# Kernel optimization log

Measured on AMD Instinct MI355X. Metric: run time of the kernel, lower is better.

Reference implementation:

```python
import jax, jax.numpy as jnp
import numpy as np

N_EMBD = 1024
N_HEAD = 16
HEAD_SIZE = N_EMBD // N_HEAD
D_FF = 4 * N_EMBD
B, T = 4, 2048
EPS = 1e-5


def _layernorm(x, w, b):
    mu = jnp.mean(x, axis=-1, keepdims=True)
    var = jnp.mean(jnp.square(x - mu), axis=-1, keepdims=True)
    return (x - mu) * jax.lax.rsqrt(var + EPS) * w + b


def setup_inputs() -> dict:
    key = jax.random.key(0)
    ks = jax.random.split(key, 12)
    s = 0.02
    x = jax.random.normal(ks[0], (B, T, N_EMBD), dtype=jnp.float32)
    # right-padded prefix mask: lengths in [T//2, T] -> no all-masked causal rows
    lengths = jax.random.randint(ks[1], (B,), T // 2, T + 1)
    key_padding_mask = jnp.arange(T)[None, :] < lengths[:, None]  # [B,T] bool, True=keep
    wq = jax.random.normal(ks[2], (N_EMBD, N_HEAD, HEAD_SIZE), dtype=jnp.float32) * s
    wk = jax.random.normal(ks[3], (N_EMBD, N_HEAD, HEAD_SIZE), dtype=jnp.float32) * s
    wv = jax.random.normal(ks[4], (N_EMBD, N_HEAD, HEAD_SIZE), dtype=jnp.float32) * s
    proj_w = jax.random.normal(ks[5], (N_EMBD, N_EMBD), dtype=jnp.float32) * s
    proj_b = jnp.zeros((N_EMBD,), dtype=jnp.float32)
    ff_w1 = jax.random.normal(ks[6], (N_EMBD, D_FF), dtype=jnp.float32) * s
    ff_b1 = jnp.zeros((D_FF,), dtype=jnp.float32)
    ff_w2 = jax.random.normal(ks[7], (D_FF, N_EMBD), dtype=jnp.float32) * s
    ff_b2 = jnp.zeros((N_EMBD,), dtype=jnp.float32)
    ln1_w = jnp.ones((N_EMBD,), dtype=jnp.float32)
    ln1_b = jnp.zeros((N_EMBD,), dtype=jnp.float32)
    ln2_w = jnp.ones((N_EMBD,), dtype=jnp.float32)
    ln2_b = jnp.zeros((N_EMBD,), dtype=jnp.float32)
    return dict(x=x, key_padding_mask=key_padding_mask, wq=wq, wk=wk, wv=wv,
                proj_w=proj_w, proj_b=proj_b, ff_w1=ff_w1, ff_b1=ff_b1,
                ff_w2=ff_w2, ff_b2=ff_b2, ln1_w=ln1_w, ln1_b=ln1_b,
                ln2_w=ln2_w, ln2_b=ln2_b)


def reference(x, key_padding_mask, wq, wk, wv, proj_w, proj_b,
              ff_w1, ff_b1, ff_w2, ff_b2, ln1_w, ln1_b, ln2_w, ln2_b):
    Bn, Tn, C = x.shape
    m = key_padding_mask.astype(x.dtype)  # [B,T]
    # --- attention sublayer ---
    h = _layernorm(x, ln1_w, ln1_b) * m[..., None]
    q = jnp.einsum('btc,chd->bhtd', h, wq)
    k = jnp.einsum('btc,chd->bhtd', h, wk)
    v = jnp.einsum('btc,chd->bhtd', h, wv)
    # NOTE: original scales by full embed dim C**-0.5, not head_size
    scores = jnp.einsum('bhtd,bhsd->bhts', q, k) * (C ** -0.5)
    causal = jnp.tril(jnp.ones((Tn, Tn), dtype=bool))
    mask = causal[None, None, :, :] & key_padding_mask[:, None, None, :]
    scores = jnp.where(mask, scores, -jnp.inf)
    wei = jax.nn.softmax(scores, axis=-1)
    out = jnp.einsum('bhts,bhsd->bthd', wei, v).reshape(Bn, Tn, C)
    x = x + out @ proj_w + proj_b
    # --- feedforward sublayer ---
    h2 = _layernorm(x, ln2_w, ln2_b) * m[..., None]
    ff = jax.nn.relu(h2 @ ff_w1 + ff_b1) @ ff_w2 + ff_b2
    x = (x + ff) * m[..., None]
    return x
```

## Files before the change

kernel.cpp:

```cpp
#include <hip/hip_runtime.h>
#include <math.h>

typedef float f32x4 __attribute__((ext_vector_type(4)));
typedef float f4 __attribute__((ext_vector_type(4)));
typedef __bf16 bf16x8 __attribute__((ext_vector_type(8)));
typedef __bf16 bf16x4 __attribute__((ext_vector_type(4)));

#define GLOBAL_AS __attribute__((address_space(1)))
#define LDS_AS __attribute__((address_space(3)))

__global__ __launch_bounds__(256) void mask_canon(const unsigned char* __restrict__ raw,
                                                  float* __restrict__ msk, int n) {
    int i = blockIdx.x * 256 + threadIdx.x;
    if (i >= n) return;
    unsigned int w0 = *(const unsigned int*)raw;
    float v;
    if (w0 == 0x01010101u)       v = raw[i] ? 1.f : 0.f;
    else if (w0 == 0x3f800000u)  v = ((const float*)raw)[i];
    else                         v = ((const int*)raw)[i] ? 1.f : 0.f;
    msk[i] = v;
}

__global__ __launch_bounds__(256) void lens_kernel(const float* __restrict__ msk,
                                                   float* __restrict__ lens) {
    int b = blockIdx.x, tid = threadIdx.x;
    float s = 0.f;
    for (int i = tid; i < 2048; i += 256) s += msk[b * 2048 + i];
#pragma unroll
    for (int off = 1; off < 64; off <<= 1) s += __shfl_xor(s, off);
    __shared__ float red[4];
    int wave = tid >> 6, lane = tid & 63;
    if (lane == 0) red[wave] = s;
    __syncthreads();
    if (tid == 0) lens[b] = red[0] + red[1] + red[2] + red[3];
}

__global__ __launch_bounds__(256) void tcvt(const float* __restrict__ src,
                                            __bf16* __restrict__ dst, int K, int N) {
    __shared__ float tile[32][33];
    int n0 = blockIdx.x * 32, k0 = blockIdx.y * 32;
    int tx = threadIdx.x & 31, ty = threadIdx.x >> 5;
#pragma unroll
    for (int i = 0; i < 4; ++i)
        tile[ty + 8 * i][tx] = src[(long)(k0 + ty + 8 * i) * N + n0 + tx];
    __syncthreads();
#pragma unroll
    for (int i = 0; i < 4; ++i)
        dst[(long)(n0 + ty + 8 * i) * K + k0 + tx] = (__bf16)tile[tx][ty + 8 * i];
}

__global__ __launch_bounds__(256) void ln_kernel(const float* __restrict__ x,
                                                 const float* __restrict__ w,
                                                 const float* __restrict__ bsc,
                                                 const float* __restrict__ msk,
                                                 __bf16* __restrict__ out) {
    long row = blockIdx.x;
    int tid = threadIdx.x;
    f4 xv = *(const f4*)(x + row * 1024 + tid * 4);
    float s = xv[0] + xv[1] + xv[2] + xv[3];
    float sq = xv[0] * xv[0] + xv[1] * xv[1] + xv[2] * xv[2] + xv[3] * xv[3];
#pragma unroll
    for (int off = 1; off < 64; off <<= 1) {
        s += __shfl_xor(s, off);
        sq += __shfl_xor(sq, off);
    }
    __shared__ float red[2][4];
    int wave = tid >> 6, lane = tid & 63;
    if (lane == 0) { red[0][wave] = s; red[1][wave] = sq; }
    __syncthreads();
    s = red[0][0] + red[0][1] + red[0][2] + red[0][3];
    sq = red[1][0] + red[1][1] + red[1][2] + red[1][3];
    float mu = s * (1.0f / 1024.0f);
    float var = sq * (1.0f / 1024.0f) - mu * mu;
    float rs = rsqrtf(var + 1e-5f);
    float mv = msk[row];
    f4 wv = *(const f4*)(w + tid * 4);
    f4 bv = *(const f4*)(bsc + tid * 4);
    bf16x4 ov;
#pragma unroll
    for (int j = 0; j < 4; ++j)
        ov[j] = (__bf16)(((xv[j] - mu) * rs * wv[j] + bv[j]) * mv);
    *(bf16x4*)(out + row * 1024 + tid * 4) = ov;
}

template <int EP>
__global__ __launch_bounds__(512, 2) void gemm_bt8(const __bf16* __restrict__ A,
                                                   const __bf16* __restrict__ B,
                                                   int K, int N, void* __restrict__ Cout,
                                                   const float* __restrict__ bias) {
    __shared__ __bf16 AB[2][2][256 * 64];
    int tid = threadIdx.x;
    int wave = tid >> 6, lane = tid & 63;
    int l15 = lane & 15, quad = lane >> 4;
    int r8 = l15 & 7;
    int wm = wave >> 2, wn = wave & 3;
    long rowBase = (long)blockIdx.x * 256;
    long colBase = (long)blockIdx.y * 256;
    const __bf16* Ab = A + rowBase * K;
    const __bf16* Bb = B + colBase * K;
    int srow = lane >> 3;
    int scol = ((lane & 7) ^ srow) * 8;
    f32x4 acc[8][4] = {};

#define STAGE2(DST, GB, seg0, kt_)                                                         \
    do {                                                                                   \
        _Pragma("unroll") for (int j = 0; j < 2; ++j) {                                    \
            int s_ = wave * 4 + (seg0) + j;                                                \
            const __bf16* g_ = (GB) + (long)(s_ * 8 + srow) * K + (kt_) + scol;            \
            __builtin_amdgcn_global_load_lds((const GLOBAL_AS void*)g_,                    \
                                             (LDS_AS void*)((char*)(DST) + s_ * 1024), 16, \
                                             0, 0);                                        \
        }                                                                                  \
    } while (0)

#define RDA(mh)                                                                      \
    do {                                                                             \
        _Pragma("unroll") for (int mi = 0; mi < 4; ++mi) {                           \
            int row_ = wm * 128 + (mh) * 64 + mi * 16 + l15;                         \
            af[mi][0] = *(const bf16x8*)(Ac + row_ * 64 + ((quad ^ r8) << 3));       \
            af[mi][1] = *(const bf16x8*)(Ac + row_ * 64 + (((4 + quad) ^ r8) << 3)); \
        }                                                                            \
    } while (0)

#define RDB(h)                                                                              \
    do {                                                                                    \
        _Pragma("unroll") for (int ni = 0; ni < 2; ++ni) {                                  \
            int row_ = wn * 64 + ((h) * 2 + ni) * 16 + l15;                                 \
            bfr[h][ni][0] = *(const bf16x8*)(Bc + row_ * 64 + ((quad ^ r8) << 3));          \
            bfr[h][ni][1] = *(const bf16x8*)(Bc + row_ * 64 + (((4 + quad) ^ r8) << 3));    \
        }                                                                                   \
    } while (0)

#define MM(mh, nh)                                                                          \
    do {                                                                                    \
        __builtin_amdgcn_s_setprio(1);                                                      \
        _Pragma("unroll") for (int mi = 0; mi < 4; ++mi) {                                  \
            _Pragma("unroll") for (int ni = 0; ni < 2; ++ni) {                              \
                acc[(mh) * 4 + mi][(nh) * 2 + ni] = __builtin_amdgcn_mfma_f32_16x16x32_bf16(\
                    af[mi][0], bfr[nh][ni][0], acc[(mh) * 4 + mi][(nh) * 2 + ni], 0, 0, 0); \
                acc[(mh) * 4 + mi][(nh) * 2 + ni] = __builtin_amdgcn_mfma_f32_16x16x32_bf16(\
                    af[mi][1], bfr[nh][ni][1], acc[(mh) * 4 + mi][(nh) * 2 + ni], 0, 0, 0); \
            }                                                                               \
        }                                                                                   \
        __builtin_amdgcn_s_setprio(0);                                                      \
    } while (0)

    STAGE2(&AB[0][0][0], Ab, 0, 0);
    STAGE2(&AB[0][0][0], Ab, 2, 0);
    STAGE2(&AB[0][1][0], Bb, 0, 0);
    STAGE2(&AB[0][1][0], Bb, 2, 0);

    int cur = 0;
    bf16x8 af[4][2], bfr[2][2][2];
    for (int kt = 0; kt < K; kt += 64) {
        const bool lastt = (kt + 64 >= K);
        const __bf16* Ac = &AB[cur][0][0];
        const __bf16* Bc = &AB[cur][1][0];
        __bf16* An = &AB[cur ^ 1][0][0];
        __bf16* Bn = &AB[cur ^ 1][1][0];
        if (!lastt) {
            STAGE2(An, Ab, 0, kt + 64);
            __asm__ volatile("s_waitcnt vmcnt(2)" ::: "memory");
        } else {
            __asm__ volatile("s_waitcnt vmcnt(0)" ::: "memory");
        }
        __asm__ volatile("s_barrier" ::: "memory");
        RDA(0);
        RDB(0);
        MM(0, 0);
        if (!lastt) STAGE2(An, Ab, 2, kt + 64);
        RDB(1);
        MM(0, 1);
        if (!lastt) STAGE2(Bn, Bb, 0, kt + 64);
        RDA(1);
        MM(1, 1);
        if (!lastt) STAGE2(Bn, Bb, 2, kt + 64);
        MM(1, 0);
        __asm__ volatile("s_barrier" ::: "memory");
        cur ^= 1;
    }
#undef STAGE2
#undef RDA
#undef RDB
#undef MM

#pragma unroll
    for (int mi = 0; mi < 8; ++mi) {
#pragma unroll
        for (int r = 0; r < 4; ++r) {
            long gr = rowBase + wm * 128 + mi * 16 + quad * 4 + r;
#pragma unroll
            for (int ni = 0; ni < 4; ++ni) {
                long gc = colBase + wn * 64 + ni * 16 + l15;
                float v = acc[mi][ni][r];
                if constexpr (EP == 0) {
                    ((__bf16*)Cout)[gr * N + gc] = (__bf16)v;
                } else {
                    v += bias[gc];
                    v = v > 0.f ? v : 0.f;
                    ((__bf16*)Cout)[gr * N + gc] = (__bf16)v;
                }
            }
        }
    }
}

template <int EP>
__global__ __launch_bounds__(512, 2) void gemm_bt8n(const __bf16* __restrict__ A,
                                                    const __bf16* __restrict__ B,
                                                    int K, int N, void* __restrict__ Cout,
                                                    const float* __restrict__ bias,
                                                    const float* __restrict__ resid,
                                                    const float* __restrict__ mskp) {
    __shared__ __bf16 As2[2][256 * 64];
    __shared__ __bf16 Bs2[2][128 * 64];
    int tid = threadIdx.x;
    int wave = tid >> 6, lane = tid & 63;
    int l15 = lane & 15, quad = lane >> 4;
    int r8 = l15 & 7;
    int wm = wave >> 1, wn = wave & 1;
    long rowBase = (long)blockIdx.x * 256;
    long colBase = (long)blockIdx.y * 128;
    const __bf16* Ab = A + rowBase * K;
    const __bf16* Bb = B + colBase * K;
    int srow = lane >> 3;
    int scol = ((lane & 7) ^ srow) * 8;
    f32x4 acc[4][4] = {};

#define NSTGA(DST, seg0, kt_)                                                              \
    do {                                                                                   \
        _Pragma("unroll") for (int j = 0; j < 2; ++j) {                                    \
            int s_ = wave * 4 + (seg0) + j;                                                \
            const __bf16* g_ = Ab + (long)(s_ * 8 + srow) * K + (kt_) + scol;              \
            __builtin_amdgcn_global_load_lds((const GLOBAL_AS void*)g_,                    \
                                             (LDS_AS void*)((char*)(DST) + s_ * 1024), 16, \
                                             0, 0);                                        \
        }                                                                                  \
    } while (0)

#define NSTGB(DST, kt_)                                                                    \
    do {                                                                                   \
        _Pragma("unroll") for (int j = 0; j < 2; ++j) {                                    \
            int s_ = wave * 2 + j;                                                         \
            const __bf16* g_ = Bb + (long)(s_ * 8 + srow) * K + (kt_) + scol;              \
            __builtin_amdgcn_global_load_lds((const GLOBAL_AS void*)g_,                    \
                                             (LDS_AS void*)((char*)(DST) + s_ * 1024), 16, \
                                             0, 0);                                        \
        }                                                                                  \
    } while (0)

#define NRA(H)                                                                            \
    do {                                                                                  \
        _Pragma("unroll") for (int mi = 0; mi < 2; ++mi) {                                \
            int row_ = wm * 64 + ((H) * 2 + mi) * 16 + l15;                               \
            afr[H][mi][0] = *(const bf16x8*)(Ac + row_ * 64 + ((quad ^ r8) << 3));        \
            afr[H][mi][1] = *(const bf16x8*)(Ac + row_ * 64 + (((4 + quad) ^ r8) << 3));  \
        }                                                                                 \
    } while (0)

#define NRB(H)                                                                            \
    do {                                                                                  \
        _Pragma("unroll") for (int ni = 0; ni < 2; ++ni) {                                \
            int row_ = wn * 64 + ((H) * 2 + ni) * 16 + l15;                               \
            bfr2[H][ni][0] = *(const bf16x8*)(Bc + row_ * 64 + ((quad ^ r8) << 3));       \
            bfr2[H][ni][1] = *(const bf16x8*)(Bc + row_ * 64 + (((4 + quad) ^ r8) << 3)); \
        }                                                                                 \
    } while (0)

#define NMM(AH, BH)                                                                          \
    do {                                                                                     \
        __builtin_amdgcn_s_setprio(1);                                                       \
        _Pragma("unroll") for (int mi = 0; mi < 2; ++mi) {                                   \
            _Pragma("unroll") for (int ni = 0; ni < 2; ++ni) {                               \
                acc[(AH) * 2 + mi][(BH) * 2 + ni] = __builtin_amdgcn_mfma_f32_16x16x32_bf16( \
                    afr[AH][mi][0], bfr2[BH][ni][0], acc[(AH) * 2 + mi][(BH) * 2 + ni], 0,   \
                    0, 0);                                                                   \
                acc[(AH) * 2 + mi][(BH) * 2 + ni] = __builtin_amdgcn_mfma_f32_16x16x32_bf16( \
                    afr[AH][mi][1], bfr2[BH][ni][1], acc[(AH) * 2 + mi][(BH) * 2 + ni], 0,   \
                    0, 0);                                                                   \
            }                                                                                \
        }                                                                                    \
        __builtin_amdgcn_s_setprio(0);                                                       \
    } while (0)

    NSTGA(&As2[0][0], 0, 0);
    NSTGA(&As2[0][0], 2, 0);
    NSTGB(&Bs2[0][0], 0);

    int cur = 0;
    bf16x8 afr[2][2][2], bfr2[2][2][2];
    for (int kt = 0; kt < K; kt += 64) {
        const bool lastt = (kt + 64 >= K);
        const __bf16* Ac = &As2[cur][0];
        const __bf16* Bc = &Bs2[cur][0];
        __bf16* An = &As2[cur ^ 1][0];
        __bf16* Bn = &Bs2[cur ^ 1][0];
        if (!lastt) {
            NSTGA(An, 0, kt + 64);
            __asm__ volatile("s_waitcnt vmcnt(2)" ::: "memory");
        } else {
            __asm__ volatile("s_waitcnt vmcnt(0)" ::: "memory");
        }
        __asm__ volatile("s_barrier" ::: "memory");
        NRA(0);
        NRB(0);
        NMM(0, 0);
        if (!lastt) NSTGA(An, 2, kt + 64);
        NRB(1);
        NMM(0, 1);
        if (!lastt) NSTGB(Bn, kt + 64);
        NRA(1);
        NMM(1, 1);
        NMM(1, 0);
        __asm__ volatile("s_barrier" ::: "memory");
        cur ^= 1;
    }
#undef NSTGA
#undef NSTGB
#undef NRA
#undef NRB
#undef NMM

#pragma unroll
    for (int mi = 0; mi < 4; ++mi) {
#pragma unroll
        for (int r = 0; r < 4; ++r) {
            long gr = rowBase + wm * 64 + mi * 16 + quad * 4 + r;
#pragma unroll
            for (int ni = 0; ni < 4; ++ni) {
                long gc = colBase + wn * 64 + ni * 16 + l15;
                float v = acc[mi][ni][r];
                if constexpr (EP == 2) {
                    v += bias[gc] + resid[gr * N + gc];
                    ((float*)Cout)[gr * N + gc] = v;
                } else {
                    v = (v + bias[gc] + resid[gr * N + gc]) * mskp[gr];
                    ((float*)Cout)[gr * N + gc] = v;
                }
            }
        }
    }
}

#define SWIZ(row, d) ((row) * 64 + ((((d) >> 3) ^ ((row) & 7)) << 3) + ((d) & 7))
__global__ __launch_bounds__(256, 3) void attn_kernel(const __bf16* __restrict__ qkv,
                                                      const float* __restrict__ lens,
                                                      __bf16* __restrict__ att) {
    const int T = 2048, C3 = 3072;
    int bh = blockIdx.x;
    int qt = 15 - blockIdx.y;
    int h = bh & 15, b = bh >> 4;
    int tid = threadIdx.x;
    int wave = tid >> 6, lane = tid & 63, l15 = lane & 15, quad = lane >> 4;

    __shared__ __bf16 Kl[64 * 64];
    __shared__ __bf16 Vt[64 * 64];
    __shared__ __bf16 Pl[4][32 * 64];

    long rowB = (long)b * T;
    const __bf16* kbase = qkv + rowB * C3 + 1024 + h * 64;
    const __bf16* vbase = qkv + rowB * C3 + 2048 + h * 64;
    const float scale2 = (1.0f / 32.0f) * 1.44269504088896f;

    int krow = tid >> 2, kd = (tid & 3) * 16;
    int vk = (tid & 15) * 4, vd = (tid >> 4) * 4;
    int vc8 = vk >> 3, vk7 = vk & 7;

    bf16x8 ones;
#pragma unroll
    for (int j = 0; j < 8; ++j) ones[j] = (__bf16)1.0f;

    __bf16* pw = &Pl[wave][0];
    int r8 = l15 & 7;

    int qbase = qt * 128;
    int wq0 = qbase + wave * 32;

    bf16x8 qf[2][2];
#pragma unroll
    for (int g = 0; g < 2; ++g) {
        const __bf16* qptr = qkv + (rowB + wq0 + g * 16 + l15) * C3 + h * 64;
        qf[g][0] = *(const bf16x8*)(qptr + quad * 8);
        qf[g][1] = *(const bf16x8*)(qptr + 32 + quad * 8);
    }

    f32x4 o0[4] = {}, o1[4] = {};
    f32x4 lacc0 = {}, lacc1 = {};
    int nchunk = 2 * qt + 2;
    float len = lens[b];

    bf16x8 kpre0, kpre1;
    bf16x4 vpre[4];
    {
        const __bf16* kg = kbase + (long)krow * C3 + kd;
        kpre0 = *(const bf16x8*)kg;
        kpre1 = *(const bf16x8*)(kg + 8);
#pragma unroll
        for (int j = 0; j < 4; ++j)
            vpre[j] = *(const bf16x4*)(vbase + (long)(vk + j) * C3 + vd);
    }

    for (int c = 0; c < nchunk; ++c) {
        int k0 = c * 64;
        __asm__ volatile("s_barrier" ::: "memory");
        *(bf16x8*)(&Kl[SWIZ(krow, kd)]) = kpre0;
        *(bf16x8*)(&Kl[SWIZ(krow, kd + 8)]) = kpre1;
#pragma unroll
        for (int dd = 0; dd < 4; ++dd) {
            bf16x4 w = {vpre[0][dd], vpre[1][dd], vpre[2][dd], vpre[3][dd]};
            int d = vd + dd;
            *(bf16x4*)(&Vt[d * 64 + ((vc8 ^ (d & 7)) << 3) + vk7]) = w;
        }
        if (c + 1 < nchunk) {
            int k1 = k0 + 64;
            const __bf16* kg = kbase + (long)(k1 + krow) * C3 + kd;
            kpre0 = *(const bf16x8*)kg;
            kpre1 = *(const bf16x8*)(kg + 8);
#pragma unroll
            for (int j = 0; j < 4; ++j)
                vpre[j] = *(const bf16x4*)(vbase + (long)(k1 + vk + j) * C3 + vd);
        }
        __asm__ volatile("s_waitcnt lgkmcnt(0)\n\ts_barrier" ::: "memory");

        if (k0 <= wq0 + 31) {
            f32x4 s0[4] = {}, s1[4] = {};
#pragma unroll
            for (int n = 0; n < 4; ++n) {
                int row = n * 16 + l15;
                bf16x8 kb0 = *(const bf16x8*)(&Kl[row * 64 + ((quad ^ r8) << 3)]);
                bf16x8 kb1 = *(const bf16x8*)(&Kl[row * 64 + (((4 + quad) ^ r8) << 3)]);
                s0[n] = __builtin_amdgcn_mfma_f32_16x16x32_bf16(kb0, qf[0][0], s0[n], 0, 0, 0);
                s0[n] = __builtin_amdgcn_mfma_f32_16x16x32_bf16(kb1, qf[0][1], s0[n], 0, 0, 0);
                s1[n] = __builtin_amdgcn_mfma_f32_16x16x32_bf16(kb0, qf[1][0], s1[n], 0, 0, 0);
                s1[n] = __builtin_amdgcn_mfma_f32_16x16x32_bf16(kb1, qf[1][1], s1[n], 0, 0, 0);
            }

            bool needC = (k0 + 63 > wq0);
#pragma unroll
            for (int n = 0; n < 4; ++n) {
                int c8 = n * 2 + (quad >> 1);
                int sub = (quad & 1) * 4;
                bf16x4 w0, w1;
                if (!needC) {
#pragma unroll
                    for (int r = 0; r < 4; ++r) {
                        w0[r] = (__bf16)exp2f(s0[n][r] * scale2);
                        w1[r] = (__bf16)exp2f(s1[n][r] * scale2);
                    }
                } else {
                    int kg = k0 + n * 16 + quad * 4;
                    int qg0 = wq0 + l15, qg1 = wq0 + 16 + l15;
#pragma unroll
                    for (int r = 0; r < 4; ++r) {
                        w0[r] = (kg + r <= qg0) ? (__bf16)exp2f(s0[n][r] * scale2) : (__bf16)0.f;
                        w1[r] = (kg + r <= qg1) ? (__bf16)exp2f(s1[n][r] * scale2) : (__bf16)0.f;
                    }
                }
                int wbase = l15 * 64 + ((c8 ^ r8) << 3) + sub;
                *(bf16x4*)(pw + wbase) = w0;
                *(bf16x4*)(pw + 1024 + wbase) = w1;
            }
            __asm__ volatile("s_waitcnt lgkmcnt(0)" ::: "memory");

            bf16x8 pa00 = *(const bf16x8*)(pw + l15 * 64 + ((quad ^ r8) << 3));
            bf16x8 pa01 = *(const bf16x8*)(pw + l15 * 64 + (((4 + quad) ^ r8) << 3));
            bf16x8 pa10 = *(const bf16x8*)(pw + 1024 + l15 * 64 + ((quad ^ r8) << 3));
            bf16x8 pa11 = *(const bf16x8*)(pw + 1024 + l15 * 64 + (((4 + quad) ^ r8) << 3));
#pragma unroll
            for (int nd = 0; nd < 4; ++nd) {
                int row = nd * 16 + l15;
                bf16x8 vb0 = *(const bf16x8*)(&Vt[row * 64 + ((quad ^ r8) << 3)]);
                bf16x8 vb1 = *(const bf16x8*)(&Vt[row * 64 + (((4 + quad) ^ r8) << 3)]);
                o0[nd] = __builtin_amdgcn_mfma_f32_16x16x32_bf16(pa00, vb0, o0[nd], 0, 0, 0);
                o0[nd] = __builtin_amdgcn_mfma_f32_16x16x32_bf16(pa01, vb1, o0[nd], 0, 0, 0);
                o1[nd] = __builtin_amdgcn_mfma_f32_16x16x32_bf16(pa10, vb0, o1[nd], 0, 0, 0);
                o1[nd] = __builtin_amdgcn_mfma_f32_16x16x32_bf16(pa11, vb1, o1[nd], 0, 0, 0);
            }
            lacc0 = __builtin_amdgcn_mfma_f32_16x16x32_bf16(pa00, ones, lacc0, 0, 0, 0);
            lacc0 = __builtin_amdgcn_mfma_f32_16x16x32_bf16(pa01, ones, lacc0, 0, 0, 0);
            lacc1 = __builtin_amdgcn_mfma_f32_16x16x32_bf16(pa10, ones, lacc1, 0, 0, 0);
            lacc1 = __builtin_amdgcn_mfma_f32_16x16x32_bf16(pa11, ones, lacc1, 0, 0, 0);
        }
    }

#pragma unroll
    for (int r = 0; r < 4; ++r) {
        int q0g = wq0 + quad * 4 + r;
        float inv0 = 1.0f / (lacc0[r] - fmaxf(0.f, (float)(q0g + 1) - len));
        long orow0 = rowB + q0g;
        int q1g = q0g + 16;
        float inv1 = 1.0f / (lacc1[r] - fmaxf(0.f, (float)(q1g + 1) - len));
        long orow1 = rowB + q1g;
#pragma unroll
        for (int nd = 0; nd < 4; ++nd) {
            att[orow0 * 1024 + h * 64 + nd * 16 + l15] = (__bf16)(o0[nd][r] * inv0);
            att[orow1 * 1024 + h * 64 + nd * 16 + l15] = (__bf16)(o1[nd][r] * inv1);
        }
    }
}

extern "C" void kernel_launch(void* const* d_in, const int* in_sizes, int n_in,
                              void* d_out, int out_size, void* d_ws, size_t ws_size,
                              hipStream_t stream) {
    const float* x      = (const float*)d_in[0];
    const void*  kpm    = d_in[1];
    const float* wq     = (const float*)d_in[2];
    const float* wk     = (const float*)d_in[3];
    const float* wv     = (const float*)d_in[4];
    const float* proj_w = (const float*)d_in[5];
    const float* proj_b = (const float*)d_in[6];
    const float* ff_w1  = (const float*)d_in[7];
    const float* ff_b1  = (const float*)d_in[8];
    const float* ff_w2  = (const float*)d_in[9];
    const float* ff_b2  = (const float*)d_in[10];
    const float* ln1w   = (const float*)d_in[11];
    const float* ln1b   = (const float*)d_in[12];
    const float* ln2w   = (const float*)d_in[13];
    const float* ln2b   = (const float*)d_in[14];

    char* ws = (char*)d_ws;
    size_t off = 0;
    auto take = [&](size_t bytes) -> char* {
        char* p = ws + off;
        off += (bytes + 255) & ~(size_t)255;
        return p;
    };
    float*  msk    = (float*)take(8192 * 4);
    float*  lens   = (float*)take(256);
    __bf16* wqkvT  = (__bf16*)take(3072L * 1024 * 2);
    __bf16* wprojT = (__bf16*)take(1024L * 1024 * 2);
    __bf16* wff1T  = (__bf16*)take(4096L * 1024 * 2);
    __bf16* wff2T  = (__bf16*)take(4096L * 1024 * 2);
    __bf16* h1     = (__bf16*)take(8192L * 1024 * 2);
    char*   qkv_c  = take(8192L * 3072 * 2);
    __bf16* qkvb   = (__bf16*)qkv_c;
    __bf16* attb   = (__bf16*)take(8192L * 1024 * 2);
    float*  x2     = (float*)take(8192L * 1024 * 4);
    __bf16* h2     = (__bf16*)take(8192L * 1024 * 2);
    __bf16* ffh    = (__bf16*)qkv_c;

    mask_canon<<<32, 256, 0, stream>>>((const unsigned char*)kpm, msk, 8192);
    lens_kernel<<<4, 256, 0, stream>>>(msk, lens);
    tcvt<<<dim3(32, 32), 256, 0, stream>>>(wq, wqkvT, 1024, 1024);
    tcvt<<<dim3(32, 32), 256, 0, stream>>>(wk, wqkvT + 1024L * 1024, 1024, 1024);
    tcvt<<<dim3(32, 32), 256, 0, stream>>>(wv, wqkvT + 2048L * 1024, 1024, 1024);
    tcvt<<<dim3(32, 32), 256, 0, stream>>>(proj_w, wprojT, 1024, 1024);
    tcvt<<<dim3(128, 32), 256, 0, stream>>>(ff_w1, wff1T, 1024, 4096);
    tcvt<<<dim3(32, 128), 256, 0, stream>>>(ff_w2, wff2T, 4096, 1024);

    ln_kernel<<<8192, 256, 0, stream>>>(x, ln1w, ln1b, msk, h1);
    gemm_bt8<0><<<dim3(32, 12), 512, 0, stream>>>(h1, wqkvT, 1024, 3072, qkvb, nullptr);
    attn_kernel<<<dim3(64, 16), 256, 0, stream>>>(qkvb, lens, attb);
    gemm_bt8n<2><<<dim3(32, 8), 512, 0, stream>>>(attb, wprojT, 1024, 1024, x2, proj_b, x, nullptr);
    ln_kernel<<<8192, 256, 0, stream>>>(x2, ln2w, ln2b, msk, h2);
    gemm_bt8<1><<<dim3(32, 16), 512, 0, stream>>>(h2, wff1T, 1024, 4096, ffh, ff_b1);
    gemm_bt8n<3><<<dim3(32, 8), 512, 0, stream>>>(ffh, wff2T, 4096, 1024, (float*)d_out, ff_b2, x2, msk);
}
```

Measured before the change: 506.8 us.

## Restructure GEMM main loops into barrier-phased ping-pong schedule with split LDS halves

Measured after the change: 488.6 us. -3.6%, faster.

```diff
diff --git a/kernel.cpp b/kernel.cpp
--- a/kernel.cpp
+++ b/kernel.cpp
@@ -83,12 +83,18 @@
     *(bf16x4*)(out + row * 1024 + tid * 4) = ov;
 }
 
+#define BARRIER   __asm__ volatile("s_barrier" ::: "memory")
+#define LGKM0     __asm__ volatile("s_waitcnt lgkmcnt(0)" ::: "memory")
+#define PRIO1     __builtin_amdgcn_s_setprio(1)
+#define PRIO0     __builtin_amdgcn_s_setprio(0)
+
 template <int EP>
 __global__ __launch_bounds__(512, 2) void gemm_bt8(const __bf16* __restrict__ A,
                                                    const __bf16* __restrict__ B,
                                                    int K, int N, void* __restrict__ Cout,
                                                    const float* __restrict__ bias) {
-    __shared__ __bf16 AB[2][2][256 * 64];
+    __shared__ __bf16 As[2][2][128 * 64];
+    __shared__ __bf16 Bs[2][2][128 * 64];
     int tid = threadIdx.x;
     int wave = tid >> 6, lane = tid & 63;
     int l15 = lane & 15, quad = lane >> 4;
@@ -102,38 +108,45 @@
     int scol = ((lane & 7) ^ srow) * 8;
     f32x4 acc[8][4] = {};
 
-#define STAGE2(DST, GB, seg0, kt_)                                                         \
-    do {                                                                                   \
-        _Pragma("unroll") for (int j = 0; j < 2; ++j) {                                    \
-            int s_ = wave * 4 + (seg0) + j;                                                \
-            const __bf16* g_ = (GB) + (long)(s_ * 8 + srow) * K + (kt_) + scol;            \
-            __builtin_amdgcn_global_load_lds((const GLOBAL_AS void*)g_,                    \
-                                             (LDS_AS void*)((char*)(DST) + s_ * 1024), 16, \
-                                             0, 0);                                        \
-        }                                                                                  \
-    } while (0)
-
+#define STGA(d_, h_, kt_)                                                                   \
+    do {                                                                                    \
+        _Pragma("unroll") for (int j = 0; j < 2; ++j) {                                     \
+            const __bf16* g_ = Ab + (long)((h_) * 128 + wave * 16 + j * 8 + srow) * K +     \
+                               (kt_) + scol;                                                \
+            __builtin_amdgcn_global_load_lds(                                               \
+                (const GLOBAL_AS void*)g_,                                                  \
+                (LDS_AS void*)((char*)&As[d_][h_][0] + wave * 2048 + j * 1024), 16, 0, 0);  \
+        }                                                                                   \
+    } while (0)
+#define STGB(d_, h_, kt_)                                                                   \
+    do {                                                                                    \
+        _Pragma("unroll") for (int j = 0; j < 2; ++j) {                                     \
+            const __bf16* g_ = Bb + (long)((h_) * 128 + wave * 16 + j * 8 + srow) * K +     \
+                               (kt_) + scol;                                                \
+            __builtin_amdgcn_global_load_lds(                                               \
+                (const GLOBAL_AS void*)g_,                                                  \
+                (LDS_AS void*)((char*)&Bs[d_][h_][0] + wave * 2048 + j * 1024), 16, 0, 0);  \
+        }                                                                                   \
+    } while (0)
 #define RDA(mh)                                                                      \
     do {                                                                             \
         _Pragma("unroll") for (int mi = 0; mi < 4; ++mi) {                           \
-            int row_ = wm * 128 + (mh) * 64 + mi * 16 + l15;                         \
+            int row_ = (mh) * 64 + mi * 16 + l15;                                    \
             af[mi][0] = *(const bf16x8*)(Ac + row_ * 64 + ((quad ^ r8) << 3));       \
             af[mi][1] = *(const bf16x8*)(Ac + row_ * 64 + (((4 + quad) ^ r8) << 3)); \
         }                                                                            \
     } while (0)
-
-#define RDB(h)                                                                              \
-    do {                                                                                    \
-        _Pragma("unroll") for (int ni = 0; ni < 2; ++ni) {                                  \
-            int row_ = wn * 64 + ((h) * 2 + ni) * 16 + l15;                                 \
-            bfr[h][ni][0] = *(const bf16x8*)(Bc + row_ * 64 + ((quad ^ r8) << 3));          \
-            bfr[h][ni][1] = *(const bf16x8*)(Bc + row_ * 64 + (((4 + quad) ^ r8) << 3));    \
-        }                                                                                   \
-    } while (0)
-
+#define RDB(h)                                                                           \
+    do {                                                                                 \
+        _Pragma("unroll") for (int ni = 0; ni < 2; ++ni) {                               \
+            int row_ = (wn & 1) * 64 + ((h) * 2 + ni) * 16 + l15;                        \
+            bfr[h][ni][0] = *(const bf16x8*)(Bc + row_ * 64 + ((quad ^ r8) << 3));       \
+            bfr[h][ni][1] = *(const bf16x8*)(Bc + row_ * 64 + (((4 + quad) ^ r8) << 3)); \
+        }                                                                                \
+    } while (0)
 #define MM(mh, nh)                                                                          \
     do {                                                                                    \
-        __builtin_amdgcn_s_setprio(1);                                                      \
+        PRIO1;                                                                              \
         _Pragma("unroll") for (int mi = 0; mi < 4; ++mi) {                                  \
             _Pragma("unroll") for (int ni = 0; ni < 2; ++ni) {                              \
                 acc[(mh) * 4 + mi][(nh) * 2 + ni] = __builtin_amdgcn_mfma_f32_16x16x32_bf16(\
@@ -142,44 +155,49 @@
                     af[mi][1], bfr[nh][ni][1], acc[(mh) * 4 + mi][(nh) * 2 + ni], 0, 0, 0); \
             }                                                                               \
         }                                                                                   \
-        __builtin_amdgcn_s_setprio(0);                                                      \
-    } while (0)
-
-    STAGE2(&AB[0][0][0], Ab, 0, 0);
-    STAGE2(&AB[0][0][0], Ab, 2, 0);
-    STAGE2(&AB[0][1][0], Bb, 0, 0);
-    STAGE2(&AB[0][1][0], Bb, 2, 0);
-
-    int cur = 0;
+        PRIO0;                                                                              \
+    } while (0)
+
+    const int NT = K >> 6;
+    STGA(0, 0, 0); STGA(0, 1, 0); STGB(0, 0, 0); STGB(0, 1, 0);
+    STGB(1, 0, 64); STGB(1, 1, 64);
+    __asm__ volatile("s_waitcnt vmcnt(4)" ::: "memory");
+    BARRIER;
+
     bf16x8 af[4][2], bfr[2][2][2];
-    for (int kt = 0; kt < K; kt += 64) {
-        const bool lastt = (kt + 64 >= K);
-        const __bf16* Ac = &AB[cur][0][0];
-        const __bf16* Bc = &AB[cur][1][0];
-        __bf16* An = &AB[cur ^ 1][0][0];
-        __bf16* Bn = &AB[cur ^ 1][1][0];
-        if (!lastt) {
-            STAGE2(An, Ab, 0, kt + 64);
-            __asm__ volatile("s_waitcnt vmcnt(2)" ::: "memory");
+    int kt = 0;
+    for (int t = 0; t < NT; ++t, kt += 64) {
+        int d = t & 1;
+        const __bf16* Ac = &As[d][wm][0];
+        const __bf16* Bc = &Bs[d][wn >> 1][0];
+        const bool haveA1 = (t + 1 < NT), haveB2 = (t + 2 < NT);
+        RDA(0); RDB(0);
+        if (haveA1) STGA(d ^ 1, 0, kt + 64);
+        BARRIER; LGKM0;
+        MM(0, 0);
+        BARRIER;
+        RDB(1);
+        if (haveA1) STGA(d ^ 1, 1, kt + 64);
+        BARRIER; LGKM0;
+        MM(0, 1);
+        BARRIER;
+        RDA(1);
+        if (haveB2) STGB(d, 0, kt + 128);
+        BARRIER; LGKM0;
+        MM(1, 1);
+        BARRIER;
+        if (haveB2) {
+            STGB(d, 1, kt + 128);
+            __asm__ volatile("s_waitcnt vmcnt(4)" ::: "memory");
         } else {
             __asm__ volatile("s_waitcnt vmcnt(0)" ::: "memory");
         }
-        __asm__ volatile("s_barrier" ::: "memory");
-        RDA(0);
-        RDB(0);
-        MM(0, 0);
-        if (!lastt) STAGE2(An, Ab, 2, kt + 64);
-        RDB(1);
-        MM(0, 1);
-        if (!lastt) STAGE2(Bn, Bb, 0, kt + 64);
-        RDA(1);
-        MM(1, 1);
-        if (!lastt) STAGE2(Bn, Bb, 2, kt + 64);
+        BARRIER;
         MM(1, 0);
-        __asm__ volatile("s_barrier" ::: "memory");
-        cur ^= 1;
-    }
-#undef STAGE2
+        BARRIER;
+    }
+#undef STGA
+#undef STGB
 #undef RDA
 #undef RDB
 #undef MM
@@ -212,8 +230,8 @@
                                                     const float* __restrict__ bias,
                                                     const float* __restrict__ resid,
                                                     const float* __restrict__ mskp) {
-    __shared__ __bf16 As2[2][256 * 64];
-    __shared__ __bf16 Bs2[2][128 * 64];
+    __shared__ __bf16 As2[2][2][128 * 64];
+    __shared__ __bf16 Bs2[2][2][64 * 64];
     int tid = threadIdx.x;
     int wave = tid >> 6, lane = tid & 63;
     int l15 = lane & 15, quad = lane >> 4;
@@ -227,49 +245,42 @@
     int scol = ((lane & 7) ^ srow) * 8;
     f32x4 acc[4][4] = {};
 
-#define NSTGA(DST, seg0, kt_)                                                              \
-    do {                                                                                   \
-        _Pragma("unroll") for (int j = 0; j < 2; ++j) {                                    \
-            int s_ = wave * 4 + (seg0) + j;                                                \
-            const __bf16* g_ = Ab + (long)(s_ * 8 + srow) * K + (kt_) + scol;              \
-            __builtin_amdgcn_global_load_lds((const GLOBAL_AS void*)g_,                    \
-                                             (LDS_AS void*)((char*)(DST) + s_ * 1024), 16, \
-                                             0, 0);                                        \
-        }                                                                                  \
-    } while (0)
-
-#define NSTGB(DST, kt_)                                                                    \
-    do {                                                                                   \
-        _Pragma("unroll") for (int j = 0; j < 2; ++j) {                                    \
-            int s_ = wave * 2 + j;                                                         \
-            const __bf16* g_ = Bb + (long)(s_ * 8 + srow) * K + (kt_) + scol;              \
-            __builtin_amdgcn_global_load_lds((const GLOBAL_AS void*)g_,                    \
-                                             (LDS_AS void*)((char*)(DST) + s_ * 1024), 16, \
-                                             0, 0);                                        \
-        }                                                                                  \
-    } while (0)
-
-#define NRA(H)                                                                            \
-    do {                                                                                  \
-        _Pragma("unroll") for (int mi = 0; mi < 2; ++mi) {                                \
-            int row_ = wm * 64 + ((H) * 2 + mi) * 16 + l15;                               \
-            afr[H][mi][0] = *(const bf16x8*)(Ac + row_ * 64 + ((quad ^ r8) << 3));        \
-            afr[H][mi][1] = *(const bf16x8*)(Ac + row_ * 64 + (((4 + quad) ^ r8) << 3));  \
-        }                                                                                 \
-    } while (0)
-
+#define NSTGA(d_, h_, kt_)                                                                  \
+    do {                                                                                    \
+        _Pragma("unroll") for (int j = 0; j < 2; ++j) {                                     \
+            const __bf16* g_ = Ab + (long)((h_) * 128 + wave * 16 + j * 8 + srow) * K +     \
+                               (kt_) + scol;                                                \
+            __builtin_amdgcn_global_load_lds(                                               \
+                (const GLOBAL_AS void*)g_,                                                  \
+                (LDS_AS void*)((char*)&As2[d_][h_][0] + wave * 2048 + j * 1024), 16, 0, 0); \
+        }                                                                                   \
+    } while (0)
+#define NSTGB(d_, h_, kt_)                                                                  \
+    do {                                                                                    \
+        const __bf16* g_ = Bb + (long)((h_) * 64 + wave * 8 + srow) * K + (kt_) + scol;     \
+        __builtin_amdgcn_global_load_lds(                                                   \
+            (const GLOBAL_AS void*)g_,                                                      \
+            (LDS_AS void*)((char*)&Bs2[d_][h_][0] + wave * 1024), 16, 0, 0);                \
+    } while (0)
+#define NRA(H)                                                                           \
+    do {                                                                                 \
+        _Pragma("unroll") for (int mi = 0; mi < 2; ++mi) {                               \
+            int row_ = (wm & 1) * 64 + ((H) * 2 + mi) * 16 + l15;                        \
+            afr[H][mi][0] = *(const bf16x8*)(Ac + row_ * 64 + ((quad ^ r8) << 3));       \
+            afr[H][mi][1] = *(const bf16x8*)(Ac + row_ * 64 + (((4 + quad) ^ r8) << 3)); \
+        }                                                                                \
+    } while (0)
 #define NRB(H)                                                                            \
     do {                                                                                  \
         _Pragma("unroll") for (int ni = 0; ni < 2; ++ni) {                                \
-            int row_ = wn * 64 + ((H) * 2 + ni) * 16 + l15;                               \
+            int row_ = ((H) * 2 + ni) * 16 + l15;                                         \
             bfr2[H][ni][0] = *(const bf16x8*)(Bc + row_ * 64 + ((quad ^ r8) << 3));       \
             bfr2[H][ni][1] = *(const bf16x8*)(Bc + row_ * 64 + (((4 + quad) ^ r8) << 3)); \
         }                                                                                 \
     } while (0)
-
 #define NMM(AH, BH)                                                                          \
     do {                                                                                     \
-        __builtin_amdgcn_s_setprio(1);                                                       \
+        PRIO1;                                                                               \
         _Pragma("unroll") for (int mi = 0; mi < 2; ++mi) {                                   \
             _Pragma("unroll") for (int ni = 0; ni < 2; ++ni) {                               \
                 acc[(AH) * 2 + mi][(BH) * 2 + ni] = __builtin_amdgcn_mfma_f32_16x16x32_bf16( \
@@ -280,40 +291,46 @@
                     0, 0);                                                                   \
             }                                                                                \
         }                                                                                    \
-        __builtin_amdgcn_s_setprio(0);                                                       \
-    } while (0)
-
-    NSTGA(&As2[0][0], 0, 0);
-    NSTGA(&As2[0][0], 2, 0);
-    NSTGB(&Bs2[0][0], 0);
-
-    int cur = 0;
+        PRIO0;                                                                               \
+    } while (0)
+
+    const int NT = K >> 6;
+    NSTGA(0, 0, 0); NSTGA(0, 1, 0); NSTGB(0, 0, 0); NSTGB(0, 1, 0);
+    NSTGB(1, 0, 64); NSTGB(1, 1, 64);
+    __asm__ volatile("s_waitcnt vmcnt(2)" ::: "memory");
+    BARRIER;
+
     bf16x8 afr[2][2][2], bfr2[2][2][2];
-    for (int kt = 0; kt < K; kt += 64) {
-        const bool lastt = (kt + 64 >= K);
-        const __bf16* Ac = &As2[cur][0];
-        const __bf16* Bc = &Bs2[cur][0];
-        __bf16* An = &As2[cur ^ 1][0];
-        __bf16* Bn = &Bs2[cur ^ 1][0];
-        if (!lastt) {
-            NSTGA(An, 0, kt + 64);
+    int kt = 0;
+    for (int t = 0; t < NT; ++t, kt += 64) {
+        int d = t & 1;
+        const __bf16* Ac = &As2[d][wm >> 1][0];
+        const __bf16* Bc = &Bs2[d][wn][0];
+        const bool haveA1 = (t + 1 < NT), haveB2 = (t + 2 < NT);
+        NRA(0); NRB(0);
+        if (haveA1) NSTGA(d ^ 1, 0, kt + 64);
+        BARRIER; LGKM0;
+        NMM(0, 0);
+        BARRIER;
+        NRB(1);
+        if (haveA1) NSTGA(d ^ 1, 1, kt + 64);
+        BARRIER; LGKM0;
+        NMM(0, 1);
+        BARRIER;
+        NRA(1);
+        if (haveB2) NSTGB(d, 0, kt + 128);
+        BARRIER; LGKM0;
+        NMM(1, 1);
+        BARRIER;
+        if (haveB2) {
+            NSTGB(d, 1, kt + 128);
             __asm__ volatile("s_waitcnt vmcnt(2)" ::: "memory");
         } else {
             __asm__ volatile("s_waitcnt vmcnt(0)" ::: "memory");
         }
-        __asm__ volatile("s_barrier" ::: "memory");
-        NRA(0);
-        NRB(0);
-        NMM(0, 0);
-        if (!lastt) NSTGA(An, 2, kt + 64);
-        NRB(1);
-        NMM(0, 1);
-        if (!lastt) NSTGB(Bn, kt + 64);
-        NRA(1);
-        NMM(1, 1);
+        BARRIER;
         NMM(1, 0);
-        __asm__ volatile("s_barrier" ::: "memory");
-        cur ^= 1;
+        BARRIER;
     }
 #undef NSTGA
 #undef NSTGB
```
